# Performance work log

Hardware: AMD Instinct MI355X
Metric: run time of the kernel (lower is better)

Reference implementation:

```python
import jax, jax.numpy as jnp
import numpy as np

B = 8192         # graphs per batch
NPG = 39         # nodes per graph (from 4560 = 40*(105+9))
N = B * NPG      # total nodes
DEG = 8          # avg degree
E = N * DEG      # total edges
NEG_SLOPE = 0.2


def _glorot(key, shape):
    fan = sum(shape) if len(shape) > 1 else shape[0] + 1
    s = jnp.sqrt(6.0 / fan)
    return jax.random.uniform(key, shape, jnp.float32, -s, s)


def setup_inputs() -> dict:
    key = jax.random.key(0)
    ks = jax.random.split(key, 32)
    x = jax.random.normal(ks[0], (N, 1), jnp.float32)
    # edges constrained within each graph
    epg = NPG * DEG
    off = jnp.repeat(jnp.arange(B, dtype=jnp.int64) * NPG, epg)
    src = jax.random.randint(ks[1], (B * epg,), 0, NPG, jnp.int64) + off
    dst = jax.random.randint(ks[2], (B * epg,), 0, NPG, jnp.int64) + off
    edge_index = jnp.stack([src, dst], 0)
    batch_ids = jnp.repeat(jnp.arange(B, dtype=jnp.int64), NPG)
    dims = [(1, 8), (8, 64), (64, 32), (32, 9)]
    p = {}
    ki = 3
    for li, (fi, fo) in enumerate(dims, 1):
        p[f'W{li}'] = _glorot(ks[ki], (fi, fo)); ki += 1
        p[f'as{li}'] = _glorot(ks[ki], (fo,)); ki += 1
        p[f'ad{li}'] = _glorot(ks[ki], (fo,)); ki += 1
        p[f'b{li}'] = jnp.zeros((fo,), jnp.float32)
    p['lw1'] = _glorot(ks[ki], (4560, 1024)); ki += 1
    p['lb1'] = jnp.zeros((1024,), jnp.float32)
    p['lw2'] = _glorot(ks[ki], (1024, 128)); ki += 1
    p['lb2'] = jnp.zeros((128,), jnp.float32)
    p['lw3'] = _glorot(ks[ki], (128, 9)); ki += 1
    p['lb3'] = jnp.zeros((9,), jnp.float32)
    return {'x': x, 'edge_index': edge_index, 'batch_ids': batch_ids, **p}


def gat_layer(x, src, dst, W, a_s, a_d, b):
    # PyG GATConv, heads=1: h=xW; e_ij = LeakyReLU(a_s.h[src]+a_d.h[dst]);
    # softmax per destination node; out = sum_j alpha * h[src] + bias
    h = x @ W                                   # [N, Fo]
    s_n = h @ a_s                               # [N]
    d_n = h @ a_d                               # [N]
    e = jax.nn.leaky_relu(s_n[src] + d_n[dst], NEG_SLOPE)   # [E+N]
    m = jax.ops.segment_max(e, dst, num_segments=N)
    w = jnp.exp(e - m[dst])
    denom = jax.ops.segment_sum(w, dst, num_segments=N)
    alpha = w / (denom[dst] + 1e-16)
    out = jax.ops.segment_sum(h[src] * alpha[:, None], dst, num_segments=N)
    return out + b


def reference(x, edge_index, batch_ids, W1, as1, ad1, b1, W2, as2, ad2, b2,
              W3, as3, ad3, b3, W4, as4, ad4, b4, lw1, lb1, lw2, lb2, lw3, lb3):
    # add self-loops (PyG GATConv default)
    sl = jnp.arange(N, dtype=edge_index.dtype)
    src = jnp.concatenate([edge_index[0], sl])
    dst = jnp.concatenate([edge_index[1], sl])
    pool = lambda h: jax.ops.segment_max(h, batch_ids, num_segments=B)

    x0 = x.reshape(-1, 1)
    res = x0.reshape(B, -1)
    out0 = pool(x0)
    h1 = jax.nn.relu(gat_layer(x0, src, dst, W1, as1, ad1, b1))
    res1, out1 = h1.reshape(B, -1), pool(h1)
    h2 = jax.nn.relu(gat_layer(h1, src, dst, W2, as2, ad2, b2))
    res2, out2 = h2.reshape(B, -1), pool(h2)
    h3 = jax.nn.relu(gat_layer(h2, src, dst, W3, as3, ad3, b3))
    res3, out3 = h3.reshape(B, -1), pool(h3)
    h4 = jax.nn.relu(gat_layer(h3, src, dst, W4, as4, ad4, b4))
    res4, out4 = h4.reshape(B, -1), pool(h4)

    f = jnp.concatenate([res, res1, res2, res3, res4,
                         out0, out1, out2, out3, out4], axis=1)  # [B, 4560]
    f = jax.nn.relu(f @ lw1 + lb1)
    f = jax.nn.relu(f @ lw2 + lb2)
    return f @ lw3 + lb3
```

## Files before the change

kernel.cpp:

```cpp
#include <hip/hip_runtime.h>

#define NPG   39
#define NGRAPH 8192
#define EPG   312
#define EDG   351
#define E0    2555904
#define FDIM  4560
#define KP    4608

typedef __bf16 bf16x8 __attribute__((ext_vector_type(8)));
typedef float  f32x4  __attribute__((ext_vector_type(4)));

__device__ __forceinline__ unsigned short f2b(float f) {
  unsigned int u = __float_as_uint(f);
  u += 0x7fffu + ((u >> 16) & 1u);
  return (unsigned short)(u >> 16);
}
__device__ __forceinline__ unsigned int pk2(float lo, float hi) {
  return (unsigned int)f2b(lo) | ((unsigned int)f2b(hi) << 16);
}
__device__ __forceinline__ float b2f(unsigned short u) {
  return __uint_as_float((unsigned int)u << 16);
}
__device__ __forceinline__ void wsync() {
  asm volatile("s_waitcnt lgkmcnt(0)" ::: "memory");
}
__device__ __forceinline__ void gsync() {
  asm volatile("s_waitcnt vmcnt(0) lgkmcnt(0)" ::: "memory");
}

__shared__ alignas(16) unsigned short Htb[32 * 64];
__shared__ alignas(16) unsigned short alf16[40 * 64];
__shared__ float sn[40];
__shared__ float dn[48];
__shared__ unsigned char csr_src[EDG + 1];
__shared__ unsigned short csr_ptr[NPG + 1];

template<int Fi, int Fo, int KPAD, int KT1, int NT, int HALVES,
         int DT, int SCOL, int DCOL, int INSRC, int OUTDST, bool GSYNC>
__device__ __forceinline__ void layerM(float x0,
                                       const unsigned short* __restrict__ Wb,
                                       const float* __restrict__ W1,
                                       const float* __restrict__ as1,
                                       const float* __restrict__ ad1,
                                       const float* __restrict__ bias,
                                       unsigned short* __restrict__ f_row,
                                       int in_off, int res_off, int out_off,
                                       int lane) {
  constexpr int NTH = NT / HALVES;
  constexpr int RMASK = (Fi >= 16) ? (Fi / 8 - 1) : 0;
  constexpr int WMASK = (Fo >= 16) ? (Fo / 8 - 1) : 0;
  constexpr int VW  = (HALVES == 2) ? 32 : Fo;
  constexpr bool SWZST = (VW == 32);
  const int r15 = lane & 15, g = lane >> 4;
  const f32x4 z = {0.f, 0.f, 0.f, 0.f};
  const uint4 z4 = {0u, 0u, 0u, 0u};

  f32x4 c1[3][NT];

  if constexpr (Fi == 1) {
    float was = 0.f, wad = 0.f;
#pragma unroll
    for (int o = 0; o < 8; ++o) { float w = W1[o]; was += w * as1[o]; wad += w * ad1[o]; }
    if (lane < NPG) {
      sn[lane] = x0 * was; dn[lane] = x0 * wad;
#pragma unroll
      for (int o = 0; o < 8; ++o) {
        int idx = o * 64 + ((((lane >> 3) ^ (o & 7)) << 3)) + (lane & 7);
        Htb[idx] = f2b(x0 * W1[o]);
      }
    }
  } else {
    if constexpr (GSYNC) gsync();
    f32x4 cd[3];
#pragma unroll
    for (int mt = 0; mt < 3; ++mt) cd[mt] = z;
#pragma unroll
    for (int mt = 0; mt < 3; ++mt)
#pragma unroll
      for (int nt = 0; nt < NT; ++nt) c1[mt][nt] = z;
#pragma unroll
    for (int kt = 0; kt < KT1; ++kt) {
      bf16x8 aF[3];
#pragma unroll
      for (int mt = 0; mt < 3; ++mt) {
        int row = 16 * mt + r15;
        if constexpr (INSRC == 2) {
          row = (row > 39) ? 39 : row;
          aF[mt] = *(const bf16x8*)&f_row[in_off + row * Fi + kt * 32 + g * 8];
        } else {
          aF[mt] = *(const bf16x8*)&alf16[row * Fi + (((kt * 4 + g) ^ (row & RMASK)) << 3)];
        }
      }
      if constexpr (DT >= NT) {
        bf16x8 bD = *(const bf16x8*)&Wb[(16 * DT + r15) * KPAD + kt * 32 + g * 8];
#pragma unroll
        for (int mt = 0; mt < 3; ++mt)
          cd[mt] = __builtin_amdgcn_mfma_f32_16x16x32_bf16(aF[mt], bD, cd[mt], 0, 0, 0);
      }
#pragma unroll
      for (int nt = 0; nt < NT; ++nt) {
        bf16x8 bW = *(const bf16x8*)&Wb[(16 * nt + r15) * KPAD + kt * 32 + g * 8];
#pragma unroll
        for (int mt = 0; mt < 3; ++mt)
          c1[mt][nt] = __builtin_amdgcn_mfma_f32_16x16x32_bf16(aF[mt], bW, c1[mt][nt], 0, 0, 0);
      }
    }
#pragma unroll
    for (int mt = 0; mt < 3; ++mt)
#pragma unroll
      for (int v = 0; v < 4; ++v) {
        float base = (DT >= NT) ? cd[mt][v] : c1[mt][DT][v];
        float t = base + __shfl_xor(base, 4);
        int r = 16 * mt + g * 4 + v;
        if (r15 == SCOL && r < NPG) sn[r] = t;
        if (r15 == DCOL && r < NPG) dn[r] = t;
      }
  }
  wsync();

#pragma unroll
  for (int i = 0; i < 5; ++i) *(uint4*)&alf16[lane * 8 + i * 512] = z4;
  wsync();

  if (lane < NPG) {
    int rs = csr_ptr[lane], re = csr_ptr[lane + 1];
    float dv = dn[lane];
    float m = -3.4e38f;
    for (int k = rs; k < re; ++k) {
      float e = sn[csr_src[k]] + dv;
      e = (e >= 0.f) ? e : 0.2f * e;
      m = fmaxf(m, e);
    }
    float den = 0.f;
    for (int k = rs; k < re; ++k) {
      int s = csr_src[k];
      float e = sn[s] + dv;
      e = (e >= 0.f) ? e : 0.2f * e;
      float w = __expf(e - m);
      int idx = lane * 64 + ((((s >> 3) ^ (lane & 7)) << 3)) + (s & 7);
      float cur = b2f(alf16[idx]);
      unsigned short nb = f2b(cur + w);
      alf16[idx] = nb;
      den += b2f(nb) - cur;
    }
    dn[lane] = 1.f / (den + 1e-16f);
  }
  wsync();

  float invr[3][4];
#pragma unroll
  for (int mt = 0; mt < 3; ++mt)
#pragma unroll
    for (int v = 0; v < 4; ++v) invr[mt][v] = dn[16 * mt + g * 4 + v];

  float pool_[NT];
#pragma unroll
  for (int s = 0; s < NT; ++s) pool_[s] = 0.f;

#pragma unroll
  for (int h = 0; h < HALVES; ++h) {
    const int colbase = (HALVES == 2) ? 32 * h : 0;
    if constexpr (Fi > 1) {
#pragma unroll
      for (int tl = 0; tl < NTH; ++tl) {
        int p = r15 + 16 * tl;
#pragma unroll
        for (int mt = 0; mt < 3; ++mt) {
          uint2 w;
          w.x = pk2(c1[mt][h * NTH + tl][0], c1[mt][h * NTH + tl][1]);
          w.y = pk2(c1[mt][h * NTH + tl][2], c1[mt][h * NTH + tl][3]);
          int idx = p * 64 + (((2 * mt + (g >> 1)) ^ (p & 7)) << 3) + (g & 1) * 4;
          *(uint2*)&Htb[idx] = w;
        }
      }
    }
    wsync();
    f32x4 c2[3][NTH];
#pragma unroll
    for (int mt = 0; mt < 3; ++mt)
#pragma unroll
      for (int tl = 0; tl < NTH; ++tl) c2[mt][tl] = z;
#pragma unroll
    for (int kt = 0; kt < 2; ++kt) {
      bf16x8 aA[3];
#pragma unroll
      for (int mt = 0; mt < 3; ++mt) {
        int row = 16 * mt + r15;
        aA[mt] = *(const bf16x8*)&alf16[row * 64 + ((((4 * kt + g) ^ (row & 7))) << 3)];
      }
#pragma unroll
      for (int tl = 0; tl < NTH; ++tl) {
        int p = r15 + 16 * tl;
        bf16x8 bH = *(const bf16x8*)&Htb[p * 64 + ((((4 * kt + g) ^ (p & 7))) << 3)];
#pragma unroll
        for (int mt = 0; mt < 3; ++mt)
          c2[mt][tl] = __builtin_amdgcn_mfma_f32_16x16x32_bf16(aA[mt], bH, c2[mt][tl], 0, 0, 0);
      }
    }
#pragma unroll
    for (int tl = 0; tl < NTH; ++tl) {
      int c = r15 + 16 * (h * NTH + tl);
      float bv = (c < Fo) ? bias[c] : 0.f;
#pragma unroll
      for (int mt = 0; mt < 3; ++mt)
#pragma unroll
        for (int v = 0; v < 4; ++v) {
          int r = 16 * mt + g * 4 + v;
          float val = fmaxf(c2[mt][tl][v] * invr[mt][v] + bv, 0.f);
          if (r < NPG && c < Fo) {
            if constexpr (OUTDST == 1) {
              alf16[r * Fo + ((((c >> 3) ^ (r & WMASK)) << 3) | (c & 7))] = f2b(val);
            } else {
              int sc = c - colbase;
              int so = SWZST ? ((sc >> 3) ^ ((r >> 2) & 3)) : (sc >> 3);
              Htb[r * VW + (so << 3) + (sc & 7)] = f2b(val);
            }
            pool_[h * NTH + tl] = fmaxf(pool_[h * NTH + tl], val);
          }
        }
    }
    wsync();

    if constexpr (OUTDST == 1) {
      if constexpr (Fo == 8) {
        if (lane < NPG)
          *(uint4*)&f_row[res_off + lane * 8] = *(const uint4*)&alf16[lane * 8];
      } else {
        for (int j = lane; j < NPG * 4; j += 64) {
          int r = j >> 2, o = j & 3;
          *(uint4*)&f_row[res_off + r * 32 + 8 * o] =
              *(const uint4*)&alf16[r * 32 + ((o ^ (r & 3)) << 3)];
        }
      }
    } else if constexpr (Fo == 9) {
      for (int j = lane; j < 43; j += 64)
        *(uint4*)&f_row[res_off + j * 8] = *(const uint4*)&Htb[j * 8];
      if (lane < 7) f_row[res_off + 344 + lane] = Htb[344 + lane];
    } else {
      for (int j = lane; j < NPG * 4; j += 64) {
        int r = j >> 2, o = j & 3;
        int so = o ^ ((r >> 2) & 3);
        *(uint4*)&f_row[res_off + r * Fo + colbase + 8 * o] =
            *(const uint4*)&Htb[r * VW + 8 * so];
      }
    }
    wsync();
  }

#pragma unroll
  for (int s = 0; s < NT; ++s) {
    float pv = pool_[s];
    pv = fmaxf(pv, __shfl_xor(pv, 16));
    pv = fmaxf(pv, __shfl_xor(pv, 32));
    int c = r15 + 16 * s;
    if (g == 0 && c < Fo) f_row[out_off + c] = f2b(pv);
  }
}

__global__ __launch_bounds__(64, 4) void gat_fused(
    const float* __restrict__ x, const int* __restrict__ ei,
    const float* __restrict__ W1, const float* __restrict__ as1, const float* __restrict__ ad1,
    const float* __restrict__ b1, const float* __restrict__ b2,
    const float* __restrict__ b3, const float* __restrict__ b4,
    const unsigned short* __restrict__ Wb,
    unsigned short* __restrict__ f) {
  const int b = blockIdx.x;
  const int lane = threadIdx.x;
  const int base = b * NPG;
  const int* srcg = ei + (size_t)b * EPG;
  const int* dstg = ei + E0 + (size_t)b * EPG;
  unsigned short* f_row = f + (size_t)b * KP;
  int* cnt = (int*)sn;
  const uint4 z4 = {0u, 0u, 0u, 0u};

#pragma unroll
  for (int i = 0; i < 4; ++i) *(uint4*)&Htb[lane * 8 + i * 512] = z4;

  float xv = 0.f;
  if (lane < NPG) {
    xv = x[(size_t)base + lane];
    f_row[lane] = f2b(xv);
  }
  if (lane == 0) f_row[39] = 0;
  if (lane < KP - 4561) f_row[4561 + lane] = 0;
  float mx = (lane < NPG) ? xv : -3.4e38f;
#pragma unroll
  for (int st = 1; st < 64; st <<= 1) { float t = __shfl_xor(mx, st); mx = fmaxf(mx, t); }
  if (lane == 0) f_row[4447] = f2b(mx);
  if (lane < NPG) cnt[lane] = 1;
  wsync();

  int es[5], ed[5];
#pragma unroll
  for (int it = 0; it < 5; ++it) {
    int e = lane + 64 * it;
    if (e < EPG) {
      int s = srcg[e] - base, d = dstg[e] - base;
      s = min(max(s, 0), NPG - 1);
      d = min(max(d, 0), NPG - 1);
      es[it] = s; ed[it] = d;
      atomicAdd(&cnt[d], 1);
    } else { es[it] = -1; ed[it] = 0; }
  }
  wsync();

  int c = (lane < NPG) ? cnt[lane] : 0;
  int v = c;
#pragma unroll
  for (int off = 1; off < 64; off <<= 1) { int t = __shfl_up(v, off); if (lane >= off) v += t; }
  int excl = v - c;
  if (lane < NPG) csr_ptr[lane] = (unsigned short)excl;
  if (lane == NPG - 1) csr_ptr[NPG] = (unsigned short)EDG;
  wsync();
  if (lane < NPG) cnt[lane] = excl;
  wsync();

  if (lane < NPG) { int p = atomicAdd(&cnt[lane], 1); csr_src[p] = (unsigned char)lane; }
#pragma unroll
  for (int it = 0; it < 5; ++it) {
    if (es[it] >= 0) {
      int p = atomicAdd(&cnt[ed[it]], 1);
      p = min(p, EDG - 1);
      csr_src[p] = (unsigned char)es[it];
    }
  }
  wsync();

  const unsigned short* Wb2 = Wb;
  const unsigned short* Wb3 = Wb + 2560;
  const unsigned short* Wb4 = Wb + 5632;

  layerM< 1,  8,  0,  0,  1,  1,  0,  0,  0,   0,    1,  false>(xv, nullptr, W1, as1, ad1, b1, f_row, 0,    40,   4448, lane);
  layerM< 8, 64, 32,  1,  4,  2,  4,  0,  1,   1,    0,  false>(0.f, Wb2, nullptr, nullptr, nullptr, b2, f_row, 0,    352,  4456, lane);
  layerM<64, 32, 64,  2,  2,  1,  2,  0,  1,   2,    1,  true >(0.f, Wb3, nullptr, nullptr, nullptr, b3, f_row, 352,  2848, 4520, lane);
  layerM<32,  9, 32,  1,  1,  1,  0, 10, 11,   1,    0,  false>(0.f, Wb4, nullptr, nullptr, nullptr, b4, f_row, 0,    4096, 4552, lane);
}

__global__ __launch_bounds__(256) void prep_wb(
    const float* __restrict__ W2, const float* __restrict__ as2, const float* __restrict__ ad2,
    const float* __restrict__ W3, const float* __restrict__ as3, const float* __restrict__ ad3,
    const float* __restrict__ W4, const float* __restrict__ as4, const float* __restrict__ ad4,
    unsigned short* __restrict__ Wb) {
  const int tid = threadIdx.x;
  for (int i = tid; i < 80 * 32; i += 256) {
    int o = i >> 5, k = i & 31; float v = 0.f;
    if (k < 8) {
      if (o < 64) v = W2[k * 64 + o];
      else if (o == 64 || o == 68) { float s = 0; for (int j = 0; j < 64; ++j) s += W2[k * 64 + j] * as2[j];
        float hi = b2f(f2b(s)); v = (o == 64) ? hi : (s - hi); }
      else if (o == 65 || o == 69) { float s = 0; for (int j = 0; j < 64; ++j) s += W2[k * 64 + j] * ad2[j];
        float hi = b2f(f2b(s)); v = (o == 65) ? hi : (s - hi); }
    }
    Wb[i] = f2b(v);
  }
  for (int i = tid; i < 48 * 64; i += 256) {
    int o = i >> 6, k = i & 63; float v = 0.f;
    if (o < 32) v = W3[k * 32 + o];
    else if (o == 32 || o == 36) { float s = 0; for (int j = 0; j < 32; ++j) s += W3[k * 32 + j] * as3[j];
      float hi = b2f(f2b(s)); v = (o == 32) ? hi : (s - hi); }
    else if (o == 33 || o == 37) { float s = 0; for (int j = 0; j < 32; ++j) s += W3[k * 32 + j] * ad3[j];
      float hi = b2f(f2b(s)); v = (o == 33) ? hi : (s - hi); }
    Wb[2560 + i] = f2b(v);
  }
  for (int i = tid; i < 16 * 32; i += 256) {
    int o = i >> 5, k = i & 31; float v = 0.f;
    if (o < 9) v = W4[k * 9 + o];
    else if (o == 10 || o == 14) { float s = 0; for (int j = 0; j < 9; ++j) s += W4[k * 9 + j] * as4[j];
      float hi = b2f(f2b(s)); v = (o == 10) ? hi : (s - hi); }
    else if (o == 11 || o == 15) { float s = 0; for (int j = 0; j < 9; ++j) s += W4[k * 9 + j] * ad4[j];
      float hi = b2f(f2b(s)); v = (o == 11) ? hi : (s - hi); }
    Wb[5632 + i] = f2b(v);
  }
}

template<bool PERM>
__global__ __launch_bounds__(256) void tcast(const float* __restrict__ in,
                                             unsigned short* __restrict__ out,
                                             int K, int NN, int Kpad) {
  __shared__ float tile[64 * 65];
  const int k0 = blockIdx.x * 64, n0 = blockIdx.y * 64;
  const int tid = threadIdx.x;
#pragma unroll
  for (int i = 0; i < 16; ++i) {
    int idx = i * 256 + tid;
    int r = idx >> 6, c = idx & 63;
    int k = k0 + r;
    int ko;
    if constexpr (PERM) {
      ko = (k < 39) ? k : ((k == 39 || k > FDIM) ? -1 : k - 1);
    } else {
      ko = (k < K) ? k : -1;
    }
    tile[r * 65 + c] = (ko >= 0) ? in[(size_t)ko * NN + n0 + c] : 0.f;
  }
  __syncthreads();
#pragma unroll
  for (int i = 0; i < 16; ++i) {
    int idx = i * 256 + tid;
    int r = idx >> 6, c = idx & 63;
    out[(size_t)(n0 + r) * Kpad + k0 + c] = f2b(tile[c * 65 + r]);
  }
}

template<bool OUT_BF16>
__global__ __launch_bounds__(256) void mfma_gemm(const unsigned short* __restrict__ A,
    const unsigned short* __restrict__ Bt, unsigned short* __restrict__ Cb,
    float* __restrict__ Cf, const float* __restrict__ bias, int K, int N, int gridN) {
  __shared__ alignas(16) unsigned short As[2][128 * 64];
  __shared__ alignas(16) unsigned short Bs[2][128 * 64];
  const int tid = threadIdx.x;
  const int lane = tid & 63;
  const int wave = tid >> 6;
  const int wy = wave >> 1, wx = wave & 1;

  const int wg = blockIdx.x;
  const int xcd = wg & 7, idx = wg >> 3;
  const int mpr = (int)(gridDim.x >> 3) / gridN;
  const int m_local = idx / gridN;
  const int n = idx - m_local * gridN;
  const int m0 = (xcd * mpr + m_local) * 128;
  const int n0 = n * 128;

  f32x4 acc[4][4];
  const f32x4 z = {0.f, 0.f, 0.f, 0.f};
#pragma unroll
  for (int i = 0; i < 4; ++i)
#pragma unroll
    for (int j = 0; j < 4; ++j) acc[i][j] = z;

  const int srow = lane >> 3;
  const int sch  = (lane & 7) ^ srow;
  const int q    = lane >> 4;
  const int rm   = lane & 15;

#define STAGE(buf, kk0)                                                              \
  {                                                                                  \
    _Pragma("unroll")                                                                \
    for (int t = 0; t < 4; ++t) {                                                    \
      int r0 = wave * 32 + t * 8;                                                    \
      const unsigned short* ga = A  + (size_t)(m0 + r0 + srow) * K + (kk0) + sch * 8;\
      const unsigned short* gb = Bt + (size_t)(n0 + r0 + srow) * K + (kk0) + sch * 8;\
      __builtin_amdgcn_global_load_lds(                                              \
          (const __attribute__((address_space(1))) unsigned int*)(const void*)ga,    \
          (__attribute__((address_space(3))) unsigned int*)(void*)&As[buf][r0 * 64], \
          16, 0, 0);                                                                 \
      __builtin_amdgcn_global_load_lds(                                              \
          (const __attribute__((address_space(1))) unsigned int*)(const void*)gb,    \
          (__attribute__((address_space(3))) unsigned int*)(void*)&Bs[buf][r0 * 64], \
          16, 0, 0);                                                                 \
    }                                                                                \
  }

  STAGE(0, 0);
  int cur = 0;
  for (int k0 = 0; k0 < K; k0 += 64) {
    if (k0 + 64 < K) {
      STAGE(cur ^ 1, k0 + 64);
      asm volatile("s_waitcnt vmcnt(8)" ::: "memory");
    } else {
      asm volatile("s_waitcnt vmcnt(0)" ::: "memory");
    }
    __builtin_amdgcn_s_barrier();
#pragma unroll
    for (int kk = 0; kk < 2; ++kk) {
      bf16x8 af[4], bfr[4];
#pragma unroll
      for (int i = 0; i < 4; ++i) {
        int ra = wy * 64 + i * 16 + rm;
        int rb = wx * 64 + i * 16 + rm;
        af[i]  = *(const bf16x8*)&As[cur][ra * 64 + (((kk * 4 + q) ^ (ra & 7)) << 3)];
        bfr[i] = *(const bf16x8*)&Bs[cur][rb * 64 + (((kk * 4 + q) ^ (rb & 7)) << 3)];
      }
#pragma unroll
      for (int i = 0; i < 4; ++i)
#pragma unroll
        for (int j = 0; j < 4; ++j)
          acc[i][j] = __builtin_amdgcn_mfma_f32_16x16x32_bf16(af[i], bfr[j], acc[i][j], 0, 0, 0);
    }
    __builtin_amdgcn_s_barrier();
    cur ^= 1;
  }
#undef STAGE

  const int q4 = (lane >> 4) * 4;
#pragma unroll
  for (int i = 0; i < 4; ++i) {
#pragma unroll
    for (int j = 0; j < 4; ++j) {
      int row = m0 + wy * 64 + i * 16 + q4;
      int col = n0 + wx * 64 + j * 16 + rm;
      float bv = bias[col];
#pragma unroll
      for (int v = 0; v < 4; ++v) {
        float val = fmaxf(acc[i][j][v] + bv, 0.f);
        if constexpr (OUT_BF16) Cb[(size_t)(row + v) * N + col] = f2b(val);
        else                    Cf[(size_t)(row + v) * N + col] = val;
      }
    }
  }
}

__global__ __launch_bounds__(256) void mlp3(const float* __restrict__ g2,
                                            const float* __restrict__ w3,
                                            const float* __restrict__ b3,
                                            float* __restrict__ out) {
  __shared__ float gs[64 * 130];
  __shared__ float ws3[128 * 9];
  const int r0 = blockIdx.x * 64;
  const int tid = threadIdx.x;
  for (int i = tid; i < 64 * 128; i += 256)
    gs[(i >> 7) * 130 + (i & 127)] = g2[(size_t)r0 * 128 + i];
  for (int i = tid; i < 128 * 9; i += 256) ws3[i] = w3[i];
  __syncthreads();
  for (int idx = tid; idx < 64 * 9; idx += 256) {
    int r = idx / 9, c = idx - r * 9;
    float acc = b3[c];
#pragma unroll 8
    for (int k = 0; k < 128; ++k) acc += gs[r * 130 + k] * ws3[k * 9 + c];
    out[(size_t)(r0 + r) * 9 + c] = acc;
  }
}

extern "C" void kernel_launch(void* const* d_in, const int* in_sizes, int n_in,
                              void* d_out, int out_size, void* d_ws, size_t ws_size,
                              hipStream_t stream) {
  const float* x   = (const float*)d_in[0];
  const int*   ei  = (const int*)d_in[1];
  const float* W1  = (const float*)d_in[3];
  const float* as1 = (const float*)d_in[4];
  const float* ad1 = (const float*)d_in[5];
  const float* b1  = (const float*)d_in[6];
  const float* W2  = (const float*)d_in[7];
  const float* as2 = (const float*)d_in[8];
  const float* ad2 = (const float*)d_in[9];
  const float* b2  = (const float*)d_in[10];
  const float* W3  = (const float*)d_in[11];
  const float* as3 = (const float*)d_in[12];
  const float* ad3 = (const float*)d_in[13];
  const float* b3  = (const float*)d_in[14];
  const float* W4  = (const float*)d_in[15];
  const float* as4 = (const float*)d_in[16];
  const float* ad4 = (const float*)d_in[17];
  const float* b4  = (const float*)d_in[18];
  const float* lw1 = (const float*)d_in[19];
  const float* lb1 = (const float*)d_in[20];
  const float* lw2 = (const float*)d_in[21];
  const float* lb2 = (const float*)d_in[22];
  const float* lw3 = (const float*)d_in[23];
  const float* lb3 = (const float*)d_in[24];
  float* out = (float*)d_out;

  unsigned short* f   = (unsigned short*)d_ws;
  unsigned short* w1t = f   + (size_t)NGRAPH * KP;
  unsigned short* w2t = w1t + (size_t)1024 * KP;
  unsigned short* g1  = w2t + (size_t)128 * 1024;
  float*          g2  = (float*)(g1 + (size_t)NGRAPH * 1024);
  unsigned short* Wb  = g1;

  prep_wb<<<1, 256, 0, stream>>>(W2, as2, ad2, W3, as3, ad3, W4, as4, ad4, Wb);
  tcast<true ><<<dim3(KP / 64, 1024 / 64), 256, 0, stream>>>(lw1, w1t, FDIM, 1024, KP);
  tcast<false><<<dim3(1024 / 64, 128 / 64), 256, 0, stream>>>(lw2, w2t, 1024, 128, 1024);

  gat_fused<<<NGRAPH, 64, 0, stream>>>(x, ei, W1, as1, ad1,
      b1, b2, b3, b4, Wb, f);

  mfma_gemm<true ><<<512, 256, 0, stream>>>(
      f, w1t, g1, nullptr, lb1, KP, 1024, 8);
  mfma_gemm<false><<<64, 256, 0, stream>>>(
      g1, w2t, nullptr, g2, lb2, 1024, 128, 1);

  mlp3<<<NGRAPH / 64, 256, 0, stream>>>(g2, lw3, lb3, out);
}
```

Measured before the change: 210.7 us.

## Fuse second and third MLP layers, use global softmax max bound, set MFMA priority

Replaces the 128-wide GEMM plus separate fp32 mlp3 kernel with one kernel that computes layer 2 with double-buffered LDS loads, keeps the ReLU output in LDS as bf16, and applies the 128x9 final layer with MFMA. This removes the g2 round trip and a launch. In the GAT kernel, the per-node softmax max loop is replaced by one wave-wide upper bound (max src + max dst score), which skips a pass over the edges. It also raises wave priority around the MFMA loops. The shared max bound can cause underflow for nodes whose scores sit far below it, and the final layer now runs in bf16.

```diff
diff --git a/kernel.cpp b/kernel.cpp
--- a/kernel.cpp
+++ b/kernel.cpp
@@ -79,6 +79,7 @@
     for (int mt = 0; mt < 3; ++mt)
 #pragma unroll
       for (int nt = 0; nt < NT; ++nt) c1[mt][nt] = z;
+    __builtin_amdgcn_s_setprio(1);
 #pragma unroll
     for (int kt = 0; kt < KT1; ++kt) {
       bf16x8 aF[3];
@@ -106,6 +107,7 @@
           c1[mt][nt] = __builtin_amdgcn_mfma_f32_16x16x32_bf16(aF[mt], bW, c1[mt][nt], 0, 0, 0);
       }
     }
+    __builtin_amdgcn_s_setprio(0);
 #pragma unroll
     for (int mt = 0; mt < 3; ++mt)
 #pragma unroll
@@ -119,6 +121,16 @@
   }
   wsync();
 
+  float svm = (lane < NPG) ? sn[lane] : -3.4e38f;
+  float dvm = (lane < NPG) ? dn[lane] : -3.4e38f;
+#pragma unroll
+  for (int st = 1; st < 64; st <<= 1) {
+    svm = fmaxf(svm, __shfl_xor(svm, st));
+    dvm = fmaxf(dvm, __shfl_xor(dvm, st));
+  }
+  float mg = svm + dvm;
+  mg = (mg >= 0.f) ? mg : 0.2f * mg;
+
 #pragma unroll
   for (int i = 0; i < 5; ++i) *(uint4*)&alf16[lane * 8 + i * 512] = z4;
   wsync();
@@ -126,18 +138,12 @@
   if (lane < NPG) {
     int rs = csr_ptr[lane], re = csr_ptr[lane + 1];
     float dv = dn[lane];
-    float m = -3.4e38f;
-    for (int k = rs; k < re; ++k) {
-      float e = sn[csr_src[k]] + dv;
-      e = (e >= 0.f) ? e : 0.2f * e;
-      m = fmaxf(m, e);
-    }
     float den = 0.f;
     for (int k = rs; k < re; ++k) {
       int s = csr_src[k];
       float e = sn[s] + dv;
       e = (e >= 0.f) ? e : 0.2f * e;
-      float w = __expf(e - m);
+      float w = __expf(e - mg);
       int idx = lane * 64 + ((((s >> 3) ^ (lane & 7)) << 3)) + (s & 7);
       float cur = b2f(alf16[idx]);
       unsigned short nb = f2b(cur + w);
@@ -181,6 +187,7 @@
     for (int mt = 0; mt < 3; ++mt)
 #pragma unroll
       for (int tl = 0; tl < NTH; ++tl) c2[mt][tl] = z;
+    __builtin_amdgcn_s_setprio(1);
 #pragma unroll
     for (int kt = 0; kt < 2; ++kt) {
       bf16x8 aA[3];
@@ -198,6 +205,7 @@
           c2[mt][tl] = __builtin_amdgcn_mfma_f32_16x16x32_bf16(aA[mt], bH, c2[mt][tl], 0, 0, 0);
       }
     }
+    __builtin_amdgcn_s_setprio(0);
 #pragma unroll
     for (int tl = 0; tl < NTH; ++tl) {
       int c = r15 + 16 * (h * NTH + tl);
@@ -341,6 +349,7 @@
     const float* __restrict__ W2, const float* __restrict__ as2, const float* __restrict__ ad2,
     const float* __restrict__ W3, const float* __restrict__ as3, const float* __restrict__ ad3,
     const float* __restrict__ W4, const float* __restrict__ as4, const float* __restrict__ ad4,
+    const float* __restrict__ w3mlp,
     unsigned short* __restrict__ Wb) {
   const int tid = threadIdx.x;
   for (int i = tid; i < 80 * 32; i += 256) {
@@ -371,6 +380,10 @@
     else if (o == 11 || o == 15) { float s = 0; for (int j = 0; j < 9; ++j) s += W4[k * 9 + j] * ad4[j];
       float hi = b2f(f2b(s)); v = (o == 11) ? hi : (s - hi); }
     Wb[5632 + i] = f2b(v);
+  }
+  for (int i = tid; i < 16 * 128; i += 256) {
+    int c = i >> 7, k = i & 127;
+    Wb[6144 + i] = f2b((c < 9) ? w3mlp[k * 9 + c] : 0.f);
   }
 }
 
@@ -501,24 +514,121 @@
   }
 }
 
-__global__ __launch_bounds__(256) void mlp3(const float* __restrict__ g2,
-                                            const float* __restrict__ w3,
-                                            const float* __restrict__ b3,
-                                            float* __restrict__ out) {
-  __shared__ float gs[64 * 130];
-  __shared__ float ws3[128 * 9];
-  const int r0 = blockIdx.x * 64;
+__global__ __launch_bounds__(256) void gemm2_fused(const unsigned short* __restrict__ A,
+    const unsigned short* __restrict__ Bt, const unsigned short* __restrict__ w3b,
+    const float* __restrict__ bias2, const float* __restrict__ b3,
+    float* __restrict__ out) {
+  __shared__ alignas(16) unsigned short As[2][128 * 64];
+  __shared__ alignas(16) unsigned short Bs[2][128 * 64];
   const int tid = threadIdx.x;
-  for (int i = tid; i < 64 * 128; i += 256)
-    gs[(i >> 7) * 130 + (i & 127)] = g2[(size_t)r0 * 128 + i];
-  for (int i = tid; i < 128 * 9; i += 256) ws3[i] = w3[i];
+  const int lane = tid & 63;
+  const int wave = tid >> 6;
+  const int wy = wave >> 1, wx = wave & 1;
+  const int m0 = blockIdx.x * 128;
+  const int K = 1024;
+
+  f32x4 acc[4][4];
+  const f32x4 z = {0.f, 0.f, 0.f, 0.f};
+#pragma unroll
+  for (int i = 0; i < 4; ++i)
+#pragma unroll
+    for (int j = 0; j < 4; ++j) acc[i][j] = z;
+
+  const int srow = lane >> 3;
+  const int sch  = (lane & 7) ^ srow;
+  const int q    = lane >> 4;
+  const int rm   = lane & 15;
+
+#define STAGE2(buf, kk0)                                                             \
+  {                                                                                  \
+    _Pragma("unroll")                                                                \
+    for (int t = 0; t < 4; ++t) {                                                    \
+      int r0 = wave * 32 + t * 8;                                                    \
+      const unsigned short* ga = A  + (size_t)(m0 + r0 + srow) * K + (kk0) + sch * 8;\
+      const unsigned short* gb = Bt + (size_t)(r0 + srow) * K + (kk0) + sch * 8;     \
+      __builtin_amdgcn_global_load_lds(                                              \
+          (const __attribute__((address_space(1))) unsigned int*)(const void*)ga,    \
+          (__attribute__((address_space(3))) unsigned int*)(void*)&As[buf][r0 * 64], \
+          16, 0, 0);                                                                 \
+      __builtin_amdgcn_global_load_lds(                                              \
+          (const __attribute__((address_space(1))) unsigned int*)(const void*)gb,    \
+          (__attribute__((address_space(3))) unsigned int*)(void*)&Bs[buf][r0 * 64], \
+          16, 0, 0);                                                                 \
+    }                                                                                \
+  }
+
+  STAGE2(0, 0);
+  int cur = 0;
+  for (int k0 = 0; k0 < K; k0 += 64) {
+    if (k0 + 64 < K) {
+      STAGE2(cur ^ 1, k0 + 64);
+      asm volatile("s_waitcnt vmcnt(8)" ::: "memory");
+    } else {
+      asm volatile("s_waitcnt vmcnt(0)" ::: "memory");
+    }
+    __builtin_amdgcn_s_barrier();
+#pragma unroll
+    for (int kk = 0; kk < 2; ++kk) {
+      bf16x8 af[4], bfr[4];
+#pragma unroll
+      for (int i = 0; i < 4; ++i) {
+        int ra = wy * 64 + i * 16 + rm;
+        int rb = wx * 64 + i * 16 + rm;
+        af[i]  = *(const bf16x8*)&As[cur][ra * 64 + (((kk * 4 + q) ^ (ra & 7)) << 3)];
+        bfr[i] = *(const bf16x8*)&Bs[cur][rb * 64 + (((kk * 4 + q) ^ (rb & 7)) << 3)];
+      }
+#pragma unroll
+      for (int i = 0; i < 4; ++i)
+#pragma unroll
+        for (int j = 0; j < 4; ++j)
+          acc[i][j] = __builtin_amdgcn_mfma_f32_16x16x32_bf16(af[i], bfr[j], acc[i][j], 0, 0, 0);
+    }
+    __builtin_amdgcn_s_barrier();
+    cur ^= 1;
+  }
+#undef STAGE2
+
+  unsigned short* gs = &As[0][0];
+  const int q4 = q * 4;
+#pragma unroll
+  for (int i = 0; i < 4; ++i) {
+#pragma unroll
+    for (int j = 0; j < 4; ++j) {
+      int cl = wx * 64 + j * 16 + rm;
+      float bv = bias2[cl];
+#pragma unroll
+      for (int v = 0; v < 4; ++v) {
+        int r = wy * 64 + i * 16 + q4 + v;
+        float val = fmaxf(acc[i][j][v] + bv, 0.f);
+        gs[r * 128 + ((((cl >> 3) ^ (r & 7)) << 3) | (cl & 7))] = f2b(val);
+      }
+    }
+  }
   __syncthreads();
-  for (int idx = tid; idx < 64 * 9; idx += 256) {
-    int r = idx / 9, c = idx - r * 9;
-    float acc = b3[c];
-#pragma unroll 8
-    for (int k = 0; k < 128; ++k) acc += gs[r * 130 + k] * ws3[k * 9 + c];
-    out[(size_t)(r0 + r) * 9 + c] = acc;
+
+  f32x4 a2[2];
+#pragma unroll
+  for (int i = 0; i < 2; ++i) a2[i] = z;
+#pragma unroll
+  for (int kt = 0; kt < 4; ++kt) {
+    bf16x8 bW3 = *(const bf16x8*)&w3b[rm * 128 + kt * 32 + q * 8];
+#pragma unroll
+    for (int i = 0; i < 2; ++i) {
+      int row = (wave * 2 + i) * 16 + rm;
+      bf16x8 aG = *(const bf16x8*)&gs[row * 128 + (((kt * 4 + q) ^ (row & 7)) << 3)];
+      a2[i] = __builtin_amdgcn_mfma_f32_16x16x32_bf16(aG, bW3, a2[i], 0, 0, 0);
+    }
+  }
+#pragma unroll
+  for (int i = 0; i < 2; ++i) {
+    if (rm < 9) {
+      float bv = b3[rm];
+#pragma unroll
+      for (int v = 0; v < 4; ++v) {
+        int row = m0 + (wave * 2 + i) * 16 + q4 + v;
+        out[(size_t)row * 9 + rm] = a2[i][v] + bv;
+      }
+    }
   }
 }
 
@@ -555,10 +665,9 @@
   unsigned short* w1t = f   + (size_t)NGRAPH * KP;
   unsigned short* w2t = w1t + (size_t)1024 * KP;
   unsigned short* g1  = w2t + (size_t)128 * 1024;
-  float*          g2  = (float*)(g1 + (size_t)NGRAPH * 1024);
-  unsigned short* Wb  = g1;
-
-  prep_wb<<<1, 256, 0, stream>>>(W2, as2, ad2, W3, as3, ad3, W4, as4, ad4, Wb);
+  unsigned short* Wb  = g1 + (size_t)NGRAPH * 1024;
+
+  prep_wb<<<1, 256, 0, stream>>>(W2, as2, ad2, W3, as3, ad3, W4, as4, ad4, lw3, Wb);
   tcast<true ><<<dim3(KP / 64, 1024 / 64), 256, 0, stream>>>(lw1, w1t, FDIM, 1024, KP);
   tcast<false><<<dim3(1024 / 64, 128 / 64), 256, 0, stream>>>(lw2, w2t, 1024, 128, 1024);
 
@@ -567,8 +676,7 @@
 
   mfma_gemm<true ><<<512, 256, 0, stream>>>(
       f, w1t, g1, nullptr, lb1, KP, 1024, 8);
-  mfma_gemm<false><<<64, 256, 0, stream>>>(
-      g1, w2t, nullptr, g2, lb2, 1024, 128, 1);
-
-  mlp3<<<NGRAPH / 64, 256, 0, stream>>>(g2, lw3, lb3, out);
-}
+
+  gemm2_fused<<<NGRAPH / 128, 256, 0, stream>>>(
+      g1, w2t, Wb + 6144, lb2, lb3, out);
+}
```

After: 193.0 us (median of 2 runs). 1.09x faster.
